# Performance work log

Hardware: AMD Instinct MI355X
Metric: run time of the kernel (lower is better)

## Reference

```python
import jax, jax.numpy as jnp
import numpy as np
import math

B, S, H, NH = 4, 1024, 1024, 16
DH = H // NH
G = 100  # native graph size


def setup_inputs() -> dict:
    key = jax.random.key(0)
    ks = jax.random.split(key, 12)
    sc = 1.0 / math.sqrt(H)
    return {
        "v": jax.random.normal(ks[0], (B, S, H), jnp.float32),
        "k": jax.random.normal(ks[1], (B, S, H), jnp.float32),
        "q": jax.random.normal(ks[2], (B, S, H), jnp.float32),
        "mask": jax.random.randint(ks[3], (B, 1, 1, S), 0, 2) == 1,
        "graph": jax.random.uniform(ks[4], (B, G, G), jnp.float32),
        "Wq": jax.random.normal(ks[5], (H, H), jnp.float32) * sc,
        "bq": jnp.zeros((H,), jnp.float32),
        "Wk": jax.random.normal(ks[6], (H, H), jnp.float32) * sc,
        "bk": jnp.zeros((H,), jnp.float32),
        "Wv": jax.random.normal(ks[7], (H, H), jnp.float32) * sc,
        "bv": jnp.zeros((H,), jnp.float32),
        "Wm": jax.random.normal(ks[8], (H, H), jnp.float32) * sc,
        "bm": jnp.zeros((H,), jnp.float32),
    }


def _heads(x, W, b):
    # [B,S,H] -> [B,NH,S,DH]
    y = x @ W + b
    return y.reshape(B, S, NH, DH).transpose(0, 2, 1, 3)


def reference(v, k, q, mask, graph, Wq, bq, Wk, bk, Wv, bv, Wm, bm):
    qh = _heads(q, Wq, bq)
    kh = _heads(k, Wk, bk)
    vh = _heads(v, Wv, bv)
    scores = jnp.einsum("bhqd,bhkd->bhqk", qh, kh) / math.sqrt(DH)
    # pad 100x100 graph to SxS (zeros outside top-left block), as in torch source
    if S > G:
        graph = jnp.zeros((B, S, S), graph.dtype).at[:, :G, :G].set(graph)
    # scores - scores*graph, then mask fill and softmax
    scores = scores - scores * graph[:, None, :, :]
    scores = jnp.where(mask, jnp.float32(-1e9), scores)
    att = jax.nn.softmax(scores, axis=-1)  # dropout is identity in eval
    out = jnp.einsum("bhqk,bhkd->bhqd", att, vh)
    out = out.transpose(0, 2, 1, 3).reshape(B, S, H)
    return out @ Wm + bm
```

## Files before the change

kernel.cpp:

```cpp
#include <hip/hip_runtime.h>
#include <hip/hip_bf16.h>
#include <cstdio>

#define S_ 1024
#define H_ 1024
#define NH_ 16
#define DH_ 64
#define G_ 100

typedef __attribute__((ext_vector_type(8))) short bf16x8;
typedef __attribute__((ext_vector_type(4))) short bf16x4;
typedef __attribute__((ext_vector_type(4))) float f32x4;

__device__ __forceinline__ f32x4 mfma16(bf16x8 a, bf16x8 b, f32x4 c) {
  return __builtin_amdgcn_mfma_f32_16x16x32_bf16(a, b, c, 0, 0, 0);
}

__device__ __forceinline__ short f2bf(float f) {
  union { float f; unsigned int i; } x;
  x.f = f;
  unsigned int r = x.i + 0x7fff + ((x.i >> 16) & 1);
  return (short)(r >> 16);
}

__device__ __forceinline__ unsigned cvtpk(float lo, float hi) {
  unsigned r;
  asm("v_cvt_pk_bf16_f32 %0, %1, %2" : "=v"(r) : "v"(lo), "v"(hi));
  return r;
}

__device__ __forceinline__ float exp2hw(float x) {
  float r;
  asm("v_exp_f32 %0, %1" : "=v"(r) : "v"(x));
  return r;
}

__device__ __forceinline__ void gload16(const void* g, void* l) {
  __builtin_amdgcn_global_load_lds(
      (const __attribute__((address_space(1))) unsigned int*)g,
      (__attribute__((address_space(3))) unsigned int*)l, 16, 0, 0);
}

__global__ __launch_bounds__(256) void transpose_w(
    const float* __restrict__ W0, const float* __restrict__ W1,
    const float* __restrict__ W2, const float* __restrict__ W3,
    short* __restrict__ T0, short* __restrict__ T1,
    short* __restrict__ T2, short* __restrict__ T3) {
  __shared__ short tile[64][72];
  const float* W = (blockIdx.z == 0) ? W0 : (blockIdx.z == 1) ? W1
                 : (blockIdx.z == 2) ? W2 : W3;
  short* T = (blockIdx.z == 0) ? T0 : (blockIdx.z == 1) ? T1
           : (blockIdx.z == 2) ? T2 : T3;
  const int t = threadIdx.x;
  const int r0 = t >> 3;
  const int c8 = (t & 7) * 8;
  const int kbase = blockIdx.x * 64, nbase = blockIdx.y * 64;
#pragma unroll
  for (int p = 0; p < 2; ++p) {
    int r = p * 32 + r0;
    const float* src = W + (size_t)(kbase + r) * H_ + nbase + c8;
    f32x4 u0 = *reinterpret_cast<const f32x4*>(src);
    f32x4 u1 = *reinterpret_cast<const f32x4*>(src + 4);
#pragma unroll
    for (int j = 0; j < 4; ++j) {
      tile[r][c8 + j] = f2bf(u0[j]);
      tile[r][c8 + 4 + j] = f2bf(u1[j]);
    }
  }
  __syncthreads();
#pragma unroll
  for (int p = 0; p < 2; ++p) {
    int r = p * 32 + r0;
    bf16x8 o;
#pragma unroll
    for (int j = 0; j < 8; ++j) o[j] = tile[c8 + j][r];
    *reinterpret_cast<bf16x8*>(T + (size_t)(nbase + r) * H_ + kbase + c8) = o;
  }
}

__global__ __launch_bounds__(256, 3) void qkv128f(
    const float* __restrict__ A0, const float* __restrict__ A1,
    const float* __restrict__ A2, const short* __restrict__ W0,
    const short* __restrict__ W1, const short* __restrict__ W2,
    const float* __restrict__ b0, const float* __restrict__ b1,
    const float* __restrict__ b2, short* __restrict__ O0,
    short* __restrict__ O1, short* __restrict__ O2) {
  __shared__ float Af[2][128 * 32];
  __shared__ short Bs[2][128 * 32];
  const int z = blockIdx.z;
  const float* A  = (z == 0) ? A0 : (z == 1) ? A1 : A2;
  const short* Bt = (z == 0) ? W0 : (z == 1) ? W1 : W2;
  const float* bias = (z == 0) ? b0 : (z == 1) ? b1 : b2;
  short* Cb = (z == 0) ? O0 : (z == 1) ? O1 : O2;
  const float scale = (z == 0) ? 0.18033688f : 1.0f;
  const int K = H_;
  const int t = threadIdx.x;
  const int l = t & 63, w = t >> 6;
  const int lr = l & 15, lg = l >> 4;
  const int lx = lr & 7;
  const int lb3 = lr & 3;
  const int wm = w >> 1, wn = w & 1;
  const int bm = blockIdx.x * 128, bn = blockIdx.y * 128;
  f32x4 acc[4][4];
#pragma unroll
  for (int i = 0; i < 4; ++i)
#pragma unroll
    for (int j = 0; j < 4; ++j) acc[i][j] = (f32x4){0.f, 0.f, 0.f, 0.f};

  const int ar = t >> 3;
  const float* Ab = A + (size_t)(bm + ar) * K + ((t & 7) ^ (ar & 7)) * 4;
  const int br = t >> 2;
  const short* Bb = Bt + (size_t)(bn + br) * K + ((t & 3) ^ (br & 3)) * 8;

  auto stage = [&](int buf, int kb) {
#pragma unroll
    for (int p = 0; p < 4; ++p)
      gload16(Ab + (size_t)p * 32 * K + kb,
              (char*)&Af[buf][0] + p * 4096 + t * 16);
#pragma unroll
    for (int p = 0; p < 2; ++p)
      gload16(Bb + (size_t)p * 64 * K + kb,
              (char*)&Bs[buf][0] + p * 4096 + t * 16);
  };

  stage(0, 0);
  __syncthreads();
  const int NT = K >> 5;
  for (int tt = 0; tt < NT; ++tt) {
    const int cur = tt & 1;
    bf16x8 af[4], bfr[4];
#pragma unroll
    for (int mi = 0; mi < 4; ++mi) {
      const int row = wm * 64 + mi * 16 + lr;
      const float* Ar = &Af[cur][row * 32];
      f32x4 alo = *reinterpret_cast<const f32x4*>(Ar + (((lg * 2) ^ lx) * 4));
      f32x4 ahi =
          *reinterpret_cast<const f32x4*>(Ar + (((lg * 2 + 1) ^ lx) * 4));
      union { unsigned u[4]; bf16x8 v; } c;
      c.u[0] = cvtpk(alo[0], alo[1]);
      c.u[1] = cvtpk(alo[2], alo[3]);
      c.u[2] = cvtpk(ahi[0], ahi[1]);
      c.u[3] = cvtpk(ahi[2], ahi[3]);
      af[mi] = c.v;
    }
#pragma unroll
    for (int ni = 0; ni < 4; ++ni) {
      const int rb = wn * 64 + ni * 16 + lr;
      bfr[ni] = *reinterpret_cast<const bf16x8*>(
          &Bs[cur][rb * 32 + ((lg ^ lb3) * 8)]);
    }
    if (tt + 1 < NT) stage(cur ^ 1, (tt + 1) << 5);
#pragma unroll
    for (int mi = 0; mi < 4; ++mi)
#pragma unroll
      for (int ni = 0; ni < 4; ++ni)
        acc[mi][ni] = mfma16(af[mi], bfr[ni], acc[mi][ni]);
    __syncthreads();
  }
#pragma unroll
  for (int mi = 0; mi < 4; ++mi)
#pragma unroll
    for (int ni = 0; ni < 4; ++ni) {
      int col = bn + wn * 64 + ni * 16 + lr;
      float bv = bias[col];
      int h = col >> 6, d = col & 63;
      if (z == 2) {
        int row0 = bm + wm * 64 + mi * 16 + lg * 4;
        int b = row0 >> 10, s0 = row0 & 1023;
        bf16x4 pk;
#pragma unroll
        for (int r = 0; r < 4; ++r) pk[r] = f2bf(acc[mi][ni][r] + bv);
        *reinterpret_cast<bf16x4*>(
            Cb + (((size_t)(b * NH_ + h)) * DH_ + d) * S_ + s0) = pk;
      } else {
#pragma unroll
        for (int r = 0; r < 4; ++r) {
          int row = bm + wm * 64 + mi * 16 + lg * 4 + r;
          int b = row >> 10, s = row & 1023;
          Cb[(((size_t)(b * NH_ + h)) * S_ + s) * DH_ + d] =
              f2bf((acc[mi][ni][r] + bv) * scale);
        }
      }
    }
}

__global__ __launch_bounds__(256) void out64(
    const short* __restrict__ A, const short* __restrict__ Bt,
    const float* __restrict__ bias, float* __restrict__ Cf) {
  __shared__ short As[64 * 64];
  __shared__ short Bs[128 * 64];
  const int K = H_, N = H_;
  const int t = threadIdx.x;
  const int l = t & 63, w = t >> 6;
  const int lr = l & 15, lg = l >> 4;
  const int lx = lr & 7;
  const int wm = w >> 1, wn = w & 1;
  const int bm = blockIdx.x * 64, bn = blockIdx.y * 128;
  f32x4 acc[2][4];
#pragma unroll
  for (int i = 0; i < 2; ++i)
#pragma unroll
    for (int j = 0; j < 4; ++j) acc[i][j] = (f32x4){0.f, 0.f, 0.f, 0.f};
  const int sr = t >> 3;
  const int ssc = ((t & 7) ^ (sr & 7)) * 8;
  const short* Ab = A + (size_t)(bm + sr) * K + ssc;
  const short* Bb = Bt + (size_t)(bn + sr) * K + ssc;
  short* la = As + t * 8;
  short* lb = Bs + t * 8;

  for (int kb = 0; kb < K; kb += 64) {
#pragma unroll
    for (int i = 0; i < 2; ++i)
      gload16(Ab + (size_t)i * 32 * K + kb, la + i * 2048);
#pragma unroll
    for (int i = 0; i < 4; ++i)
      gload16(Bb + (size_t)i * 32 * K + kb, lb + i * 2048);
    __syncthreads();
#pragma unroll
    for (int ks = 0; ks < 2; ++ks) {
      bf16x8 af[2], bfr[4];
#pragma unroll
      for (int mi = 0; mi < 2; ++mi)
        af[mi] = *reinterpret_cast<const bf16x8*>(
            &As[(wm * 32 + mi * 16 + lr) * 64 + (((ks * 4 + lg) ^ lx) * 8)]);
#pragma unroll
      for (int ni = 0; ni < 4; ++ni)
        bfr[ni] = *reinterpret_cast<const bf16x8*>(
            &Bs[(wn * 64 + ni * 16 + lr) * 64 + (((ks * 4 + lg) ^ lx) * 8)]);
#pragma unroll
      for (int mi = 0; mi < 2; ++mi)
#pragma unroll
        for (int ni = 0; ni < 4; ++ni)
          acc[mi][ni] = mfma16(af[mi], bfr[ni], acc[mi][ni]);
    }
    __syncthreads();
  }
#pragma unroll
  for (int mi = 0; mi < 2; ++mi)
#pragma unroll
    for (int ni = 0; ni < 4; ++ni) {
      int col = bn + wn * 64 + ni * 16 + lr;
      float bv = bias[col];
#pragma unroll
      for (int r = 0; r < 4; ++r) {
        int row = bm + wm * 32 + mi * 16 + lg * 4 + r;
        Cf[(size_t)row * N + col] = acc[mi][ni][r] + bv;
      }
    }
}

__global__ __launch_bounds__(256) void attn(
    const short* __restrict__ Qh, const short* __restrict__ Kh,
    const short* __restrict__ VhT, const float* __restrict__ graph,
    const int* __restrict__ mask, short* __restrict__ ctx) {
  __shared__ short Kb[64 * 64];
  __shared__ short Vb[64 * 64];
  __shared__ short P[4 * 16 * 64];
  __shared__ float maskf[S_];
  const int lin = blockIdx.x;
  const int gid = (lin & 7) * 128 + (lin >> 3);
  const int bh = gid >> 4, qt = gid & 15;
  const int b = bh >> 4, h = bh & 15;
  const int t = threadIdx.x, w = t >> 6, l = t & 63;
  const int lr = l & 15, lg = l >> 4;
  const int lx = lr & 7;
  const int q0 = qt * 64 + w * 16;
  const int qg = q0 + lr;
  short* Pw = P + w * 1024;
  const short* Qrow = Qh + ((size_t)bh * S_ + qg) * DH_;
  bf16x8 qf0 = *reinterpret_cast<const bf16x8*>(Qrow + lg * 8);
  bf16x8 qf1 = *reinterpret_cast<const bf16x8*>(Qrow + 32 + lg * 8);
  f32x4 o[4];
#pragma unroll
  for (int i = 0; i < 4; ++i) o[i] = (f32x4){0.f, 0.f, 0.f, 0.f};
  float llp = 0.f;

  const int rs = t >> 2;
  const int g0 = t & 3;
  const int sw0 = ((g0 ^ (rs & 7)) * 8);
  const int sw1 = (((g0 + 4) ^ (rs & 7)) * 8);
  const short* Ksrc = Kh + ((size_t)bh * S_ + rs) * DH_ + g0 * 8;
  const short* Vsrc = VhT + ((size_t)bh * DH_ + rs) * S_ + g0 * 8;

  {
    int4 mv = reinterpret_cast<const int4*>(mask + b * S_)[t];
    f32x4 mo;
    const float C = -16.0f;
    mo.x = mv.x ? -1.0e9f : C;
    mo.y = mv.y ? -1.0e9f : C;
    mo.z = mv.z ? -1.0e9f : C;
    mo.w = mv.w ? -1.0e9f : C;
    reinterpret_cast<f32x4*>(maskf)[t] = mo;
  }
  {
    int4 ka = *reinterpret_cast<const int4*>(Ksrc);
    int4 kb2 = *reinterpret_cast<const int4*>(Ksrc + 32);
    int4 va = *reinterpret_cast<const int4*>(Vsrc);
    int4 vb2 = *reinterpret_cast<const int4*>(Vsrc + 32);
    *reinterpret_cast<int4*>(&Kb[rs * 64 + sw0]) = ka;
    *reinterpret_cast<int4*>(&Kb[rs * 64 + sw1]) = kb2;
    *reinterpret_cast<int4*>(&Vb[rs * 64 + sw0]) = va;
    *reinterpret_cast<int4*>(&Vb[rs * 64 + sw1]) = vb2;
  }
  __syncthreads();

  for (int kc = 0; kc < S_; kc += 64) {
    const bool pf = (kc + 64 < S_);
    int4 ka, kb2, va, vb2;
    if (pf) {
      ka = *reinterpret_cast<const int4*>(Ksrc + (size_t)(kc + 64) * DH_);
      kb2 = *reinterpret_cast<const int4*>(Ksrc + (size_t)(kc + 64) * DH_ + 32);
      va = *reinterpret_cast<const int4*>(Vsrc + kc + 64);
      vb2 = *reinterpret_cast<const int4*>(Vsrc + kc + 64 + 32);
    }
    f32x4 sacc[4];
    __builtin_amdgcn_s_setprio(1);
#pragma unroll
    for (int mf = 0; mf < 4; ++mf) {
      const int rk = mf * 16 + lr;
      bf16x8 k0 = *reinterpret_cast<const bf16x8*>(
          &Kb[rk * 64 + ((lg ^ lx) * 8)]);
      bf16x8 k1 = *reinterpret_cast<const bf16x8*>(
          &Kb[rk * 64 + (((4 + lg) ^ lx) * 8)]);
      f32x4 sa = (f32x4){0.f, 0.f, 0.f, 0.f};
      sa = mfma16(k0, qf0, sa);
      sa = mfma16(k1, qf1, sa);
      sacc[mf] = sa;
    }
    __builtin_amdgcn_s_setprio(0);
    const bool gblk = (q0 < G_) && (kc < G_);
    const int pw0 = lr * 64 + (lg & 1) * 4;
#pragma unroll
    for (int mf = 0; mf < 4; ++mf) {
      f32x4 mk = *reinterpret_cast<const f32x4*>(&maskf[kc + mf * 16 + lg * 4]);
      f32x4 sa = sacc[mf];
      if (gblk) {
#pragma unroll
        for (int r = 0; r < 4; ++r) {
          int kg = kc + mf * 16 + lg * 4 + r;
          if (qg < G_ && kg < G_)
            sa[r] *= (1.f - graph[((size_t)b * G_ + qg) * G_ + kg]);
        }
      }
      float e0 = exp2hw(sa[0] + mk[0]);
      float e1 = exp2hw(sa[1] + mk[1]);
      float e2 = exp2hw(sa[2] + mk[2]);
      float e3 = exp2hw(sa[3] + mk[3]);
      llp += (e0 + e1) + (e2 + e3);
      int2 pk2;
      pk2.x = (int)cvtpk(e0, e1);
      pk2.y = (int)cvtpk(e2, e3);
      *reinterpret_cast<int2*>(
          &Pw[pw0 + (((2 * mf + (lg >> 1)) ^ lx) * 8)]) = pk2;
    }
    __builtin_amdgcn_s_setprio(1);
#pragma unroll
    for (int ks = 0; ks < 2; ++ks) {
      bf16x8 pa = *reinterpret_cast<const bf16x8*>(
          &Pw[lr * 64 + (((ks * 4 + lg) ^ lx) * 8)]);
#pragma unroll
      for (int nf = 0; nf < 4; ++nf) {
        const int rv = nf * 16 + lr;
        bf16x8 vfr = *reinterpret_cast<const bf16x8*>(
            &Vb[rv * 64 + (((ks * 4 + lg) ^ lx) * 8)]);
        o[nf] = mfma16(pa, vfr, o[nf]);
      }
    }
    __builtin_amdgcn_s_setprio(0);
    if (pf) {
      __syncthreads();
      *reinterpret_cast<int4*>(&Kb[rs * 64 + sw0]) = ka;
      *reinterpret_cast<int4*>(&Kb[rs * 64 + sw1]) = kb2;
      *reinterpret_cast<int4*>(&Vb[rs * 64 + sw0]) = va;
      *reinterpret_cast<int4*>(&Vb[rs * 64 + sw1]) = vb2;
      __syncthreads();
    }
  }
  llp += __shfl_xor(llp, 16);
  llp += __shfl_xor(llp, 32);
  float rinv[4];
#pragma unroll
  for (int r = 0; r < 4; ++r)
    rinv[r] = __builtin_amdgcn_rcpf(__shfl(llp, lg * 4 + r, 64));
#pragma unroll
  for (int nf = 0; nf < 4; ++nf)
#pragma unroll
    for (int r = 0; r < 4; ++r) {
      float val = o[nf][r] * rinv[r];
      ctx[((size_t)b * S_ + q0 + lg * 4 + r) * H_ + h * DH_ + nf * 16 + lr] =
          f2bf(val);
    }
}

extern "C" void kernel_launch(void* const* d_in, const int* in_sizes, int n_in,
                              void* d_out, int out_size, void* d_ws, size_t ws_size,
                              hipStream_t stream) {
  const int B = in_sizes[0] / (S_ * H_);
  const int M = B * S_;
  const float* v    = (const float*)d_in[0];
  const float* k    = (const float*)d_in[1];
  const float* q    = (const float*)d_in[2];
  const int*   mask = (const int*)d_in[3];
  const float* graph= (const float*)d_in[4];
  const float* Wq   = (const float*)d_in[5];
  const float* bq   = (const float*)d_in[6];
  const float* Wk   = (const float*)d_in[7];
  const float* bk   = (const float*)d_in[8];
  const float* Wv   = (const float*)d_in[9];
  const float* bv   = (const float*)d_in[10];
  const float* Wm   = (const float*)d_in[11];
  const float* bm   = (const float*)d_in[12];

  short* ws = (short*)d_ws;
  const size_t WSZ = (size_t)H_ * H_;
  const size_t TSZ = (size_t)M * H_;
  short* WqT = ws;
  short* WkT = ws + WSZ;
  short* WvT = ws + 2 * WSZ;
  short* WmT = ws + 3 * WSZ;
  short* Qh  = ws + 4 * WSZ;
  short* Kh  = Qh + TSZ;
  short* VhT = Kh + TSZ;
  short* ctx = VhT + TSZ;
  if (ws_size < (4 * WSZ + 4 * TSZ) * sizeof(short)) {
    fprintf(stderr, "kernel_launch: ws too small (%zu)\n", ws_size);
    return;
  }

  transpose_w<<<dim3(H_ / 64, H_ / 64, 4), 256, 0, stream>>>(
      Wq, Wk, Wv, Wm, WqT, WkT, WvT, WmT);
  qkv128f<<<dim3(M / 128, H_ / 128, 3), 256, 0, stream>>>(
      q, k, v, WqT, WkT, WvT, bq, bk, bv, Qh, Kh, VhT);
  attn<<<dim3(1024), 256, 0, stream>>>(Qh, Kh, VhT, graph, mask, ctx);
  out64<<<dim3(M / 64, H_ / 128), 256, 0, stream>>>(
      ctx, WmT, bm, (float*)d_out);
}
```

Measured before the change: 106.2 us.

## Double-buffer out-projection GEMM and fix LDS swizzles to avoid bank conflicts

The output-projection GEMM moves from a single-buffered 64-wide K loop to a double-buffered 32-wide K loop. The next tile's global-to-LDS loads are issued before the MFMAs so they overlap compute, and the loop needs only one barrier per step. The bf16 LDS XOR swizzle in the QKV projection and the output GEMM now uses (row>>1)&3, and the attention K/V staging alternates which half each row's threads load first, both aimed at reducing LDS bank conflicts. The risk is twice as many loop iterations in the output GEMM and a swizzle mismatch if any read and write pattern disagree.

```diff
diff --git a/kernel.cpp b/kernel.cpp
--- a/kernel.cpp
+++ b/kernel.cpp
@@ -98,7 +98,7 @@
   const int l = t & 63, w = t >> 6;
   const int lr = l & 15, lg = l >> 4;
   const int lx = lr & 7;
-  const int lb3 = lr & 3;
+  const int lk = (lr >> 1) & 3;
   const int wm = w >> 1, wn = w & 1;
   const int bm = blockIdx.x * 128, bn = blockIdx.y * 128;
   f32x4 acc[4][4];
@@ -110,7 +110,8 @@
   const int ar = t >> 3;
   const float* Ab = A + (size_t)(bm + ar) * K + ((t & 7) ^ (ar & 7)) * 4;
   const int br = t >> 2;
-  const short* Bb = Bt + (size_t)(bn + br) * K + ((t & 3) ^ (br & 3)) * 8;
+  const short* Bb =
+      Bt + (size_t)(bn + br) * K + ((t & 3) ^ ((br >> 1) & 3)) * 8;
 
   auto stage = [&](int buf, int kb) {
 #pragma unroll
@@ -147,7 +148,7 @@
     for (int ni = 0; ni < 4; ++ni) {
       const int rb = wn * 64 + ni * 16 + lr;
       bfr[ni] = *reinterpret_cast<const bf16x8*>(
-          &Bs[cur][rb * 32 + ((lg ^ lb3) * 8)]);
+          &Bs[cur][rb * 32 + ((lg ^ lk) * 8)]);
     }
     if (tt + 1 < NT) stage(cur ^ 1, (tt + 1) << 5);
 #pragma unroll
@@ -187,13 +188,13 @@
 __global__ __launch_bounds__(256) void out64(
     const short* __restrict__ A, const short* __restrict__ Bt,
     const float* __restrict__ bias, float* __restrict__ Cf) {
-  __shared__ short As[64 * 64];
-  __shared__ short Bs[128 * 64];
+  __shared__ short As[2][64 * 32];
+  __shared__ short Bs[2][128 * 32];
   const int K = H_, N = H_;
   const int t = threadIdx.x;
   const int l = t & 63, w = t >> 6;
   const int lr = l & 15, lg = l >> 4;
-  const int lx = lr & 7;
+  const int lk = (lr >> 1) & 3;
   const int wm = w >> 1, wn = w & 1;
   const int bm = blockIdx.x * 64, bn = blockIdx.y * 128;
   f32x4 acc[2][4];
@@ -201,38 +202,41 @@
   for (int i = 0; i < 2; ++i)
 #pragma unroll
     for (int j = 0; j < 4; ++j) acc[i][j] = (f32x4){0.f, 0.f, 0.f, 0.f};
-  const int sr = t >> 3;
-  const int ssc = ((t & 7) ^ (sr & 7)) * 8;
-  const short* Ab = A + (size_t)(bm + sr) * K + ssc;
-  const short* Bb = Bt + (size_t)(bn + sr) * K + ssc;
-  short* la = As + t * 8;
-  short* lb = Bs + t * 8;
-
-  for (int kb = 0; kb < K; kb += 64) {
-#pragma unroll
-    for (int i = 0; i < 2; ++i)
-      gload16(Ab + (size_t)i * 32 * K + kb, la + i * 2048);
-#pragma unroll
-    for (int i = 0; i < 4; ++i)
-      gload16(Bb + (size_t)i * 32 * K + kb, lb + i * 2048);
-    __syncthreads();
-#pragma unroll
-    for (int ks = 0; ks < 2; ++ks) {
-      bf16x8 af[2], bfr[4];
-#pragma unroll
-      for (int mi = 0; mi < 2; ++mi)
-        af[mi] = *reinterpret_cast<const bf16x8*>(
-            &As[(wm * 32 + mi * 16 + lr) * 64 + (((ks * 4 + lg) ^ lx) * 8)]);
+  const int sr = t >> 2;
+  const int ss = ((t & 3) ^ ((sr >> 1) & 3)) * 8;
+  const short* Ab = A + (size_t)(bm + sr) * K + ss;
+  const short* Bb = Bt + (size_t)(bn + sr) * K + ss;
+
+  auto stage = [&](int buf, int kb) {
+    gload16(Ab + kb, (char*)&As[buf][0] + t * 16);
+    gload16(Bb + kb, (char*)&Bs[buf][0] + t * 16);
+    gload16(Bb + (size_t)64 * K + kb, (char*)&Bs[buf][0] + 4096 + t * 16);
+  };
+
+  stage(0, 0);
+  __syncthreads();
+  const int NT = K >> 5;
+  for (int tt = 0; tt < NT; ++tt) {
+    const int cur = tt & 1;
+    bf16x8 af[2], bfr[4];
+#pragma unroll
+    for (int mi = 0; mi < 2; ++mi) {
+      const int row = wm * 32 + mi * 16 + lr;
+      af[mi] = *reinterpret_cast<const bf16x8*>(
+          &As[cur][row * 32 + ((lg ^ lk) * 8)]);
+    }
+#pragma unroll
+    for (int ni = 0; ni < 4; ++ni) {
+      const int rb = wn * 64 + ni * 16 + lr;
+      bfr[ni] = *reinterpret_cast<const bf16x8*>(
+          &Bs[cur][rb * 32 + ((lg ^ lk) * 8)]);
+    }
+    if (tt + 1 < NT) stage(cur ^ 1, (tt + 1) << 5);
+#pragma unroll
+    for (int mi = 0; mi < 2; ++mi)
 #pragma unroll
       for (int ni = 0; ni < 4; ++ni)
-        bfr[ni] = *reinterpret_cast<const bf16x8*>(
-            &Bs[(wn * 64 + ni * 16 + lr) * 64 + (((ks * 4 + lg) ^ lx) * 8)]);
-#pragma unroll
-      for (int mi = 0; mi < 2; ++mi)
-#pragma unroll
-        for (int ni = 0; ni < 4; ++ni)
-          acc[mi][ni] = mfma16(af[mi], bfr[ni], acc[mi][ni]);
-    }
+        acc[mi][ni] = mfma16(af[mi], bfr[ni], acc[mi][ni]);
     __syncthreads();
   }
 #pragma unroll
@@ -276,11 +280,14 @@
   float llp = 0.f;
 
   const int rs = t >> 2;
-  const int g0 = t & 3;
-  const int sw0 = ((g0 ^ (rs & 7)) * 8);
-  const int sw1 = (((g0 + 4) ^ (rs & 7)) * 8);
-  const short* Ksrc = Kh + ((size_t)bh * S_ + rs) * DH_ + g0 * 8;
-  const short* Vsrc = VhT + ((size_t)bh * DH_ + rs) * S_ + g0 * 8;
+  const int ga = (t & 3) + ((rs & 1) << 2);
+  const int gb = ga ^ 4;
+  const int sw0 = ((ga ^ (rs & 7)) * 8);
+  const int sw1 = ((gb ^ (rs & 7)) * 8);
+  const short* Ksrc0 = Kh + ((size_t)bh * S_ + rs) * DH_ + ga * 8;
+  const short* Ksrc1 = Kh + ((size_t)bh * S_ + rs) * DH_ + gb * 8;
+  const short* Vsrc0 = VhT + ((size_t)bh * DH_ + rs) * S_ + ga * 8;
+  const short* Vsrc1 = VhT + ((size_t)bh * DH_ + rs) * S_ + gb * 8;
 
   {
     int4 mv = reinterpret_cast<const int4*>(mask + b * S_)[t];
@@ -293,10 +300,10 @@
     reinterpret_cast<f32x4*>(maskf)[t] = mo;
   }
   {
-    int4 ka = *reinterpret_cast<const int4*>(Ksrc);
-    int4 kb2 = *reinterpret_cast<const int4*>(Ksrc + 32);
-    int4 va = *reinterpret_cast<const int4*>(Vsrc);
-    int4 vb2 = *reinterpret_cast<const int4*>(Vsrc + 32);
+    int4 ka = *reinterpret_cast<const int4*>(Ksrc0);
+    int4 kb2 = *reinterpret_cast<const int4*>(Ksrc1);
+    int4 va = *reinterpret_cast<const int4*>(Vsrc0);
+    int4 vb2 = *reinterpret_cast<const int4*>(Vsrc1);
     *reinterpret_cast<int4*>(&Kb[rs * 64 + sw0]) = ka;
     *reinterpret_cast<int4*>(&Kb[rs * 64 + sw1]) = kb2;
     *reinterpret_cast<int4*>(&Vb[rs * 64 + sw0]) = va;
@@ -308,10 +315,10 @@
     const bool pf = (kc + 64 < S_);
     int4 ka, kb2, va, vb2;
     if (pf) {
-      ka = *reinterpret_cast<const int4*>(Ksrc + (size_t)(kc + 64) * DH_);
-      kb2 = *reinterpret_cast<const int4*>(Ksrc + (size_t)(kc + 64) * DH_ + 32);
-      va = *reinterpret_cast<const int4*>(Vsrc + kc + 64);
-      vb2 = *reinterpret_cast<const int4*>(Vsrc + kc + 64 + 32);
+      ka = *reinterpret_cast<const int4*>(Ksrc0 + (size_t)(kc + 64) * DH_);
+      kb2 = *reinterpret_cast<const int4*>(Ksrc1 + (size_t)(kc + 64) * DH_);
+      va = *reinterpret_cast<const int4*>(Vsrc0 + kc + 64);
+      vb2 = *reinterpret_cast<const int4*>(Vsrc1 + kc + 64);
     }
     f32x4 sacc[4];
     __builtin_amdgcn_s_setprio(1);
```

Result: no change. 106.9 us (+0.6%).
